# Kernel optimization log

Measured on AMD Instinct MI355X. Metric: run time of the kernel, lower is better.

Reference implementation:

```python
import jax, jax.numpy as jnp
import numpy as np

NUM_EMB = 81920
EMB_DIM = 64


def setup_inputs() -> dict:
    key = jax.random.key(0)
    k1, k2 = jax.random.split(key)
    z = jax.random.normal(k1, (4, 8, 8, 8, EMB_DIM), dtype=jnp.float32)
    # faithful to nn.Embedding init: uniform(-1/K, 1/K)
    emb = jax.random.uniform(k2, (NUM_EMB, EMB_DIM), dtype=jnp.float32,
                             minval=-1.0 / NUM_EMB, maxval=1.0 / NUM_EMB)
    return {"z": z, "emb": emb}


def reference(z, emb):
    bs, h, w, d, c = z.shape
    zf = z.reshape(-1, c)  # [N, C]
    # squared euclidean distances; argmin identical to cdist argmin
    # [N, K] = ||z||^2 - 2 z.E^T + ||E||^2
    d2 = (jnp.sum(zf * zf, axis=-1, keepdims=True)
          - 2.0 * jnp.einsum('nc,kc->nk', zf, emb)
          + jnp.sum(emb * emb, axis=-1))
    idx = jnp.argmin(d2, axis=1)  # [N]
    quantized = emb[idx].reshape(bs, h, w, d, c)
    commitment_loss = jnp.mean((z - jax.lax.stop_gradient(quantized)) ** 2)
    vq_loss = jnp.mean((quantized - jax.lax.stop_gradient(z)) ** 2)
    quantized_st = z + jax.lax.stop_gradient(quantized - z)
    return quantized_st, vq_loss, commitment_loss, idx.reshape(bs, h, w, d)
```

## Files before the change

kernel.cpp:

```cpp
#include <hip/hip_runtime.h>
#include <stdint.h>

#define NQ 2048
#define KK 81920
#define CD 64
#define CAP 64
#define DMARG 1.6e-5f
#define QPB 64
#define NQBLK 32
#define NSLICE 160
#define SPX 20
#define SPB 5

#define OUT_VQ 131072
#define OUT_CM 131073
#define OUT_IDX 131074

#define WS_CNT  8192
#define WS_LOSS 32768
#define WS_CAND 33024
#define WS_ZBF  589824
#define WS_EBF  851968
#define WS_BMAX 11337728

typedef short v8s __attribute__((ext_vector_type(8)));
typedef float v4f __attribute__((ext_vector_type(4)));

__device__ __forceinline__ unsigned int f2o(float f) {
  unsigned int u = __float_as_uint(f);
  return (u & 0x80000000u) ? ~u : (u | 0x80000000u);
}
__device__ __forceinline__ float o2f(unsigned int u) {
  unsigned int v = (u & 0x80000000u) ? (u & 0x7FFFFFFFu) : ~u;
  return __uint_as_float(v);
}
__device__ __forceinline__ unsigned int bf16rne(float f) {
  unsigned int u = __float_as_uint(f);
  u = u + 0x7FFFu + ((u >> 16) & 1u);
  return u >> 16;
}

#define NZ4 32768
#define NTOT4 1343488
__global__ __launch_bounds__(256) void convert_kernel(
    const float* __restrict__ z, const float* __restrict__ emb,
    unsigned int* __restrict__ zbf, unsigned int* __restrict__ ebf,
    int* __restrict__ cnt, float* __restrict__ loss) {
  const int gid = blockIdx.x * 256 + threadIdx.x;
  if (gid < NQ) cnt[gid] = 0;
  if (gid == NQ) *loss = 0.0f;
  const int stride = gridDim.x * 256;
#pragma unroll 1
  for (int i = gid; i < NTOT4; i += stride) {
    const bool isz = (i < NZ4);
    const float4 v = isz ? ((const float4*)z)[i] : ((const float4*)emb)[i - NZ4];
    uint2 o;
    o.x = bf16rne(v.x) | (bf16rne(v.y) << 16);
    o.y = bf16rne(v.z) | (bf16rne(v.w) << 16);
    if (isz) ((uint2*)zbf)[i] = o;
    else     ((uint2*)ebf)[i - NZ4] = o;
  }
}

struct BlkMap { int q0, slice0, xcd, sgrp; };
__device__ __forceinline__ BlkMap decode_block(int bid) {
  BlkMap m;
  m.xcd = bid & 7;
  const int i = bid >> 3;
  const int qblk = i & 31;
  m.sgrp = i >> 5;
  m.q0 = qblk * QPB;
  m.slice0 = m.xcd * SPX + m.sgrp * SPB;
  return m;
}

__device__ __forceinline__ void load_B4(v8s (&Bb)[4][2],
                                        const unsigned short* __restrict__ ebf,
                                        int code0, int lrow, int quad) {
#pragma unroll
  for (int cg = 0; cg < 4; ++cg) {
    const unsigned short* er = ebf + (size_t)(code0 + cg * 16 + lrow) * CD + quad * 8;
    Bb[cg][0] = *(const v8s*)er;
    Bb[cg][1] = *(const v8s*)(er + 32);
  }
}

__global__ __launch_bounds__(256, 2) void pass1_kernel(
    const unsigned short* __restrict__ zbf, const unsigned short* __restrict__ ebf,
    unsigned int* __restrict__ bmax) {
  const int tid = threadIdx.x;
  const int wave = tid >> 6, lane = tid & 63;
  const int quad = lane >> 4, lrow = lane & 15;
  const BlkMap bm = decode_block(blockIdx.x);

  v8s A0[4], A1[4];
#pragma unroll
  for (int qg = 0; qg < 4; ++qg) {
    const unsigned short* zr = zbf + (size_t)(bm.q0 + qg * 16 + lrow) * CD + quad * 8;
    A0[qg] = *(const v8s*)zr;
    A1[qg] = *(const v8s*)(zr + 32);
  }

  float pmax[4][4];
#pragma unroll
  for (int qg = 0; qg < 4; ++qg)
#pragma unroll
    for (int r = 0; r < 4; ++r) pmax[qg][r] = -1e30f;

#pragma unroll 1
  for (int s = 0; s < SPB; ++s) {
#pragma unroll 1
    for (int h = 0; h < 2; ++h) {
      v8s B[4][2];
      load_B4(B, ebf, (bm.slice0 + s) * 512 + wave * 128 + h * 64, lrow, quad);
#pragma unroll
      for (int qg = 0; qg < 4; ++qg) {
#pragma unroll
        for (int cg = 0; cg < 4; ++cg) {
          v4f acc = {0.f, 0.f, 0.f, 0.f};
          acc = __builtin_amdgcn_mfma_f32_16x16x32_bf16(A0[qg], B[cg][0], acc, 0, 0, 0);
          acc = __builtin_amdgcn_mfma_f32_16x16x32_bf16(A1[qg], B[cg][1], acc, 0, 0, 0);
#pragma unroll
          for (int r = 0; r < 4; ++r) pmax[qg][r] = fmaxf(pmax[qg][r], acc[r]);
        }
      }
    }
  }

#pragma unroll
  for (int m = 1; m <= 8; m <<= 1)
#pragma unroll
    for (int qg = 0; qg < 4; ++qg)
#pragma unroll
      for (int r = 0; r < 4; ++r)
        pmax[qg][r] = fmaxf(pmax[qg][r], __shfl_xor(pmax[qg][r], m, 64));

  __shared__ unsigned int smax[4][QPB];
  if (lrow == 0) {
#pragma unroll
    for (int qg = 0; qg < 4; ++qg) {
      uint4 v;
      v.x = f2o(pmax[qg][0]); v.y = f2o(pmax[qg][1]);
      v.z = f2o(pmax[qg][2]); v.w = f2o(pmax[qg][3]);
      *(uint4*)&smax[wave][qg * 16 + quad * 4] = v;
    }
  }
  __syncthreads();
  if (tid < QPB) {
    unsigned int m0 = smax[0][tid], m1 = smax[1][tid];
    unsigned int m2 = smax[2][tid], m3 = smax[3][tid];
    unsigned int m01 = m0 > m1 ? m0 : m1;
    unsigned int m23 = m2 > m3 ? m2 : m3;
    bmax[(size_t)(bm.q0 + tid) * 32 + bm.xcd * 4 + bm.sgrp] = m01 > m23 ? m01 : m23;
  }
}

__global__ __launch_bounds__(256, 2) void collect_kernel(
    const unsigned short* __restrict__ zbf, const unsigned short* __restrict__ ebf,
    const unsigned int* __restrict__ bmax, int* __restrict__ cnt,
    int* __restrict__ cand) {
  const int tid = threadIdx.x;
  const int wave = tid >> 6, lane = tid & 63;
  const int quad = lane >> 4, lrow = lane & 15;
  const BlkMap bm = decode_block(blockIdx.x);

  __shared__ unsigned int qmaxl[QPB];
  if (tid < QPB) {
    const uint4* bp = (const uint4*)(bmax + (size_t)(bm.q0 + tid) * 32);
    unsigned int m = 0;
#pragma unroll
    for (int j = 0; j < 8; ++j) {
      uint4 v = bp[j];
      unsigned int a = v.x > v.y ? v.x : v.y;
      unsigned int b = v.z > v.w ? v.z : v.w;
      unsigned int c = a > b ? a : b;
      m = m > c ? m : c;
    }
    qmaxl[tid] = m;
  }

  v8s A0[4], A1[4];
#pragma unroll
  for (int qg = 0; qg < 4; ++qg) {
    const unsigned short* zr = zbf + (size_t)(bm.q0 + qg * 16 + lrow) * CD + quad * 8;
    A0[qg] = *(const v8s*)zr;
    A1[qg] = *(const v8s*)(zr + 32);
  }
  __syncthreads();
  float thr[4][4];
#pragma unroll
  for (int qg = 0; qg < 4; ++qg) {
    const uint4 tv = *(const uint4*)&qmaxl[qg * 16 + quad * 4];
    thr[qg][0] = o2f(tv.x) - DMARG; thr[qg][1] = o2f(tv.y) - DMARG;
    thr[qg][2] = o2f(tv.z) - DMARG; thr[qg][3] = o2f(tv.w) - DMARG;
  }

#pragma unroll 1
  for (int s = 0; s < SPB; ++s) {
#pragma unroll 1
    for (int h = 0; h < 2; ++h) {
      const int code0 = (bm.slice0 + s) * 512 + wave * 128 + h * 64;
      v8s B[4][2];
      load_B4(B, ebf, code0, lrow, quad);
#pragma unroll
      for (int qg = 0; qg < 4; ++qg) {
#pragma unroll
        for (int cg = 0; cg < 4; ++cg) {
          v4f acc = {0.f, 0.f, 0.f, 0.f};
          acc = __builtin_amdgcn_mfma_f32_16x16x32_bf16(A0[qg], B[cg][0], acc, 0, 0, 0);
          acc = __builtin_amdgcn_mfma_f32_16x16x32_bf16(A1[qg], B[cg][1], acc, 0, 0, 0);
          const float m01 = fmaxf(acc[0] - thr[qg][0], acc[1] - thr[qg][1]);
          const float m23 = fmaxf(acc[2] - thr[qg][2], acc[3] - thr[qg][3]);
          if (fmaxf(m01, m23) >= 0.0f) {
            const int code = code0 + cg * 16 + lrow;
#pragma unroll
            for (int r = 0; r < 4; ++r) {
              if (acc[r] >= thr[qg][r]) {
                const int q = bm.q0 + qg * 16 + quad * 4 + r;
                const int pos = atomicAdd(&cnt[q], 1);
                if (pos < CAP) cand[q * CAP + pos] = code;
              }
            }
          }
        }
      }
    }
  }
}

__device__ __forceinline__ unsigned long long exact_key(
    const float* __restrict__ emb, const float zr[CD], float zn2, int k) {
#pragma clang fp contract(off)
  float er[CD];
  const float4* ep = (const float4*)(emb + (size_t)k * CD);
#pragma unroll
  for (int j = 0; j < 16; ++j) {
    float4 v = ep[j];
    er[4 * j] = v.x; er[4 * j + 1] = v.y; er[4 * j + 2] = v.z; er[4 * j + 3] = v.w;
  }
  float acc[16];
#pragma unroll
  for (int j = 0; j < 16; ++j) acc[j] = 0.0f;
#pragma unroll
  for (int q4 = 0; q4 < 16; ++q4) {
    const int jb = 4 * (q4 & 3), cb = 4 * q4;
    acc[jb + 0] = __builtin_fmaf(er[cb + 0], zr[cb + 0], acc[jb + 0]);
    acc[jb + 1] = __builtin_fmaf(er[cb + 1], zr[cb + 1], acc[jb + 1]);
    acc[jb + 2] = __builtin_fmaf(er[cb + 2], zr[cb + 2], acc[jb + 2]);
    acc[jb + 3] = __builtin_fmaf(er[cb + 3], zr[cb + 3], acc[jb + 3]);
  }
  float b8[8], b4[4];
#pragma unroll
  for (int j = 0; j < 8; ++j) b8[j] = acc[j] + acc[j + 8];
#pragma unroll
  for (int j = 0; j < 4; ++j) b4[j] = b8[j] + b8[j + 4];
  const float dot = (b4[0] + b4[2]) + (b4[1] + b4[3]);
  const float t = zn2 - 2.0f * dot;
  return ((unsigned long long)f2o(t) << 32) | (unsigned int)k;
}

__global__ __launch_bounds__(256) void rescore_finalize_kernel(
    const float* __restrict__ z, const float* __restrict__ emb,
    const int* __restrict__ cnt, const int* __restrict__ cand,
    float* __restrict__ out, float* __restrict__ loss) {
#pragma clang fp contract(off)
  const int t = threadIdx.x;
  const int wv = t >> 6, lane = t & 63;
  const int n = blockIdx.x * 4 + wv;

  float zr[CD];
  {
    const float4* zp = (const float4*)(z + (size_t)n * CD);
#pragma unroll
    for (int i = 0; i < 16; ++i) {
      float4 v = zp[i];
      zr[4 * i] = v.x; zr[4 * i + 1] = v.y; zr[4 * i + 2] = v.z; zr[4 * i + 3] = v.w;
    }
  }
  float zn2;
  {
    float r[8];
#pragma unroll
    for (int j = 0; j < 8; ++j) r[j] = zr[j] * zr[j];
#pragma unroll
    for (int i = 8; i < CD; i += 8)
#pragma unroll
      for (int j = 0; j < 8; ++j) r[j] += zr[i + j] * zr[i + j];
    zn2 = ((r[0] + r[1]) + (r[2] + r[3])) + ((r[4] + r[5]) + (r[6] + r[7]));
  }

  const int c = cnt[n];
  unsigned long long best = ~0ull;
  if (c <= CAP) {
    if (lane < c) best = exact_key(emb, zr, zn2, cand[n * CAP + lane]);
  } else {
#pragma unroll 1
    for (int k = lane; k < KK; k += 64) {
      unsigned long long key = exact_key(emb, zr, zn2, k);
      best = (key < best) ? key : best;
    }
  }
#pragma unroll
  for (int m = 32; m; m >>= 1) {
    unsigned long long o = __shfl_xor(best, m, 64);
    best = (o < best) ? o : best;
  }
  const int idx = (int)(best & 0xFFFFFFFFull);

  const float e = emb[(size_t)idx * CD + lane];
  const float zv = z[(size_t)n * CD + lane];
  const float dst = e - zv;
  out[(size_t)n * CD + lane] = zv + dst;
  if (lane == 0) out[OUT_IDX + n] = (float)idx;
  float d = zv - e;
  float sq = d * d;
#pragma unroll
  for (int off = 32; off > 0; off >>= 1) sq += __shfl_down(sq, off, 64);
  __shared__ float part[4];
  if (lane == 0) part[wv] = sq;
  __syncthreads();
  if (t == 0) atomicAdd(loss, part[0] + part[1] + part[2] + part[3]);
}

__global__ void write_losses(const float* __restrict__ loss, float* __restrict__ out) {
  float m = *loss / (float)(NQ * CD);
  out[OUT_VQ] = m;
  out[OUT_CM] = m;
}

extern "C" void kernel_launch(void* const* d_in, const int* in_sizes, int n_in,
                              void* d_out, int out_size, void* d_ws, size_t ws_size,
                              hipStream_t stream) {
  const float* z = (const float*)d_in[0];
  const float* emb = (const float*)d_in[1];
  float* out = (float*)d_out;
  char* ws = (char*)d_ws;
  int* cnt = (int*)(ws + WS_CNT);
  float* loss = (float*)(ws + WS_LOSS);
  int* cand = (int*)(ws + WS_CAND);
  unsigned int* zbf = (unsigned int*)(ws + WS_ZBF);
  unsigned int* ebf = (unsigned int*)(ws + WS_EBF);
  unsigned int* bmax = (unsigned int*)(ws + WS_BMAX);

  convert_kernel<<<1312, 256, 0, stream>>>(z, emb, zbf, ebf, cnt, loss);
  const int nblk = NQBLK * (NSLICE / SPB);
  pass1_kernel<<<nblk, 256, 0, stream>>>(
      (const unsigned short*)zbf, (const unsigned short*)ebf, bmax);
  collect_kernel<<<nblk, 256, 0, stream>>>(
      (const unsigned short*)zbf, (const unsigned short*)ebf, bmax, cnt, cand);
  rescore_finalize_kernel<<<NQ / 4, 256, 0, stream>>>(z, emb, cnt, cand, out, loss);
  write_losses<<<1, 1, 0, stream>>>(loss, out);
}
```

Baseline: 174.1 us.

## Replace collect pass with per-chunk max and chunk-level exact rescoring

```diff
diff --git a/kernel.cpp b/kernel.cpp
--- a/kernel.cpp
+++ b/kernel.cpp
@@ -4,24 +4,22 @@
 #define NQ 2048
 #define KK 81920
 #define CD 64
-#define CAP 64
 #define DMARG 1.6e-5f
 #define QPB 64
 #define NQBLK 32
-#define NSLICE 160
 #define SPX 20
 #define SPB 5
+#define NCHUNK 640
 
 #define OUT_VQ 131072
 #define OUT_CM 131073
 #define OUT_IDX 131074
 
-#define WS_CNT  8192
-#define WS_LOSS 32768
-#define WS_CAND 33024
-#define WS_ZBF  589824
-#define WS_EBF  851968
-#define WS_BMAX 11337728
+#define WS_LOSS 0
+#define WS_TICKET 256
+#define WS_ZBF  1024
+#define WS_EBF  263168
+#define WS_CMAX 10748928
 
 typedef short v8s __attribute__((ext_vector_type(8)));
 typedef float v4f __attribute__((ext_vector_type(4)));
@@ -45,10 +43,9 @@
 __global__ __launch_bounds__(256) void convert_kernel(
     const float* __restrict__ z, const float* __restrict__ emb,
     unsigned int* __restrict__ zbf, unsigned int* __restrict__ ebf,
-    int* __restrict__ cnt, float* __restrict__ loss) {
+    float* __restrict__ loss, unsigned int* __restrict__ ticket) {
   const int gid = blockIdx.x * 256 + threadIdx.x;
-  if (gid < NQ) cnt[gid] = 0;
-  if (gid == NQ) *loss = 0.0f;
+  if (gid == 0) { *loss = 0.0f; *ticket = 0u; }
   const int stride = gridDim.x * 256;
 #pragma unroll 1
   for (int i = gid; i < NTOT4; i += stride) {
@@ -62,15 +59,15 @@
   }
 }
 
-struct BlkMap { int q0, slice0, xcd, sgrp; };
+struct BlkMap { int q0, slice0; };
 __device__ __forceinline__ BlkMap decode_block(int bid) {
   BlkMap m;
-  m.xcd = bid & 7;
+  const int xcd = bid & 7;
   const int i = bid >> 3;
   const int qblk = i & 31;
-  m.sgrp = i >> 5;
+  const int sgrp = i >> 5;
   m.q0 = qblk * QPB;
-  m.slice0 = m.xcd * SPX + m.sgrp * SPB;
+  m.slice0 = xcd * SPX + sgrp * SPB;
   return m;
 }
 
@@ -87,7 +84,7 @@
 
 __global__ __launch_bounds__(256, 2) void pass1_kernel(
     const unsigned short* __restrict__ zbf, const unsigned short* __restrict__ ebf,
-    unsigned int* __restrict__ bmax) {
+    unsigned int* __restrict__ cmax) {
   const int tid = threadIdx.x;
   const int wave = tid >> 6, lane = tid & 63;
   const int quad = lane >> 4, lrow = lane & 15;
@@ -101,14 +98,14 @@
     A1[qg] = *(const v8s*)(zr + 32);
   }
 
-  float pmax[4][4];
-#pragma unroll
-  for (int qg = 0; qg < 4; ++qg)
-#pragma unroll
-    for (int r = 0; r < 4; ++r) pmax[qg][r] = -1e30f;
-
 #pragma unroll 1
   for (int s = 0; s < SPB; ++s) {
+    float pmax[4][4];
+#pragma unroll
+    for (int qg = 0; qg < 4; ++qg)
+#pragma unroll
+      for (int r = 0; r < 4; ++r) pmax[qg][r] = -1e30f;
+
 #pragma unroll 1
     for (int h = 0; h < 2; ++h) {
       v8s B[4][2];
@@ -125,105 +122,23 @@
         }
       }
     }
-  }
-
-#pragma unroll
-  for (int m = 1; m <= 8; m <<= 1)
-#pragma unroll
-    for (int qg = 0; qg < 4; ++qg)
-#pragma unroll
-      for (int r = 0; r < 4; ++r)
-        pmax[qg][r] = fmaxf(pmax[qg][r], __shfl_xor(pmax[qg][r], m, 64));
-
-  __shared__ unsigned int smax[4][QPB];
-  if (lrow == 0) {
-#pragma unroll
-    for (int qg = 0; qg < 4; ++qg) {
-      uint4 v;
-      v.x = f2o(pmax[qg][0]); v.y = f2o(pmax[qg][1]);
-      v.z = f2o(pmax[qg][2]); v.w = f2o(pmax[qg][3]);
-      *(uint4*)&smax[wave][qg * 16 + quad * 4] = v;
-    }
-  }
-  __syncthreads();
-  if (tid < QPB) {
-    unsigned int m0 = smax[0][tid], m1 = smax[1][tid];
-    unsigned int m2 = smax[2][tid], m3 = smax[3][tid];
-    unsigned int m01 = m0 > m1 ? m0 : m1;
-    unsigned int m23 = m2 > m3 ? m2 : m3;
-    bmax[(size_t)(bm.q0 + tid) * 32 + bm.xcd * 4 + bm.sgrp] = m01 > m23 ? m01 : m23;
-  }
-}
-
-__global__ __launch_bounds__(256, 2) void collect_kernel(
-    const unsigned short* __restrict__ zbf, const unsigned short* __restrict__ ebf,
-    const unsigned int* __restrict__ bmax, int* __restrict__ cnt,
-    int* __restrict__ cand) {
-  const int tid = threadIdx.x;
-  const int wave = tid >> 6, lane = tid & 63;
-  const int quad = lane >> 4, lrow = lane & 15;
-  const BlkMap bm = decode_block(blockIdx.x);
-
-  __shared__ unsigned int qmaxl[QPB];
-  if (tid < QPB) {
-    const uint4* bp = (const uint4*)(bmax + (size_t)(bm.q0 + tid) * 32);
-    unsigned int m = 0;
-#pragma unroll
-    for (int j = 0; j < 8; ++j) {
-      uint4 v = bp[j];
-      unsigned int a = v.x > v.y ? v.x : v.y;
-      unsigned int b = v.z > v.w ? v.z : v.w;
-      unsigned int c = a > b ? a : b;
-      m = m > c ? m : c;
-    }
-    qmaxl[tid] = m;
-  }
-
-  v8s A0[4], A1[4];
-#pragma unroll
-  for (int qg = 0; qg < 4; ++qg) {
-    const unsigned short* zr = zbf + (size_t)(bm.q0 + qg * 16 + lrow) * CD + quad * 8;
-    A0[qg] = *(const v8s*)zr;
-    A1[qg] = *(const v8s*)(zr + 32);
-  }
-  __syncthreads();
-  float thr[4][4];
-#pragma unroll
-  for (int qg = 0; qg < 4; ++qg) {
-    const uint4 tv = *(const uint4*)&qmaxl[qg * 16 + quad * 4];
-    thr[qg][0] = o2f(tv.x) - DMARG; thr[qg][1] = o2f(tv.y) - DMARG;
-    thr[qg][2] = o2f(tv.z) - DMARG; thr[qg][3] = o2f(tv.w) - DMARG;
-  }
-
-#pragma unroll 1
-  for (int s = 0; s < SPB; ++s) {
-#pragma unroll 1
-    for (int h = 0; h < 2; ++h) {
-      const int code0 = (bm.slice0 + s) * 512 + wave * 128 + h * 64;
-      v8s B[4][2];
-      load_B4(B, ebf, code0, lrow, quad);
-#pragma unroll
-      for (int qg = 0; qg < 4; ++qg) {
-#pragma unroll
-        for (int cg = 0; cg < 4; ++cg) {
-          v4f acc = {0.f, 0.f, 0.f, 0.f};
-          acc = __builtin_amdgcn_mfma_f32_16x16x32_bf16(A0[qg], B[cg][0], acc, 0, 0, 0);
-          acc = __builtin_amdgcn_mfma_f32_16x16x32_bf16(A1[qg], B[cg][1], acc, 0, 0, 0);
-          const float m01 = fmaxf(acc[0] - thr[qg][0], acc[1] - thr[qg][1]);
-          const float m23 = fmaxf(acc[2] - thr[qg][2], acc[3] - thr[qg][3]);
-          if (fmaxf(m01, m23) >= 0.0f) {
-            const int code = code0 + cg * 16 + lrow;
-#pragma unroll
-            for (int r = 0; r < 4; ++r) {
-              if (acc[r] >= thr[qg][r]) {
-                const int q = bm.q0 + qg * 16 + quad * 4 + r;
-                const int pos = atomicAdd(&cnt[q], 1);
-                if (pos < CAP) cand[q * CAP + pos] = code;
-              }
-            }
-          }
-        }
-      }
+
+#pragma unroll
+    for (int m = 1; m <= 8; m <<= 1)
+#pragma unroll
+      for (int qg = 0; qg < 4; ++qg)
+#pragma unroll
+        for (int r = 0; r < 4; ++r)
+          pmax[qg][r] = fmaxf(pmax[qg][r], __shfl_xor(pmax[qg][r], m, 64));
+
+    const int ch = (bm.slice0 + s) * 4 + wave;
+    if (lrow == 0) {
+#pragma unroll
+      for (int qg = 0; qg < 4; ++qg)
+#pragma unroll
+        for (int r = 0; r < 4; ++r)
+          cmax[(size_t)(bm.q0 + qg * 16 + quad * 4 + r) * NCHUNK + ch] =
+              f2o(pmax[qg][r]);
     }
   }
 }
@@ -261,8 +176,8 @@
 
 __global__ __launch_bounds__(256) void rescore_finalize_kernel(
     const float* __restrict__ z, const float* __restrict__ emb,
-    const int* __restrict__ cnt, const int* __restrict__ cand,
-    float* __restrict__ out, float* __restrict__ loss) {
+    const unsigned int* __restrict__ cmax, float* __restrict__ out,
+    float* __restrict__ loss, unsigned int* __restrict__ ticket) {
 #pragma clang fp contract(off)
   const int t = threadIdx.x;
   const int wv = t >> 6, lane = t & 63;
@@ -289,15 +204,32 @@
     zn2 = ((r[0] + r[1]) + (r[2] + r[3])) + ((r[4] + r[5]) + (r[6] + r[7]));
   }
 
-  const int c = cnt[n];
+  const unsigned int* cm = cmax + (size_t)n * NCHUNK;
+  unsigned int val[10];
+#pragma unroll
+  for (int j = 0; j < 10; ++j) val[j] = cm[j * 64 + lane];
+  unsigned int qm = val[0];
+#pragma unroll
+  for (int j = 1; j < 10; ++j) qm = val[j] > qm ? val[j] : qm;
+#pragma unroll
+  for (int m = 32; m; m >>= 1) {
+    unsigned int o = (unsigned int)__shfl_xor((int)qm, m, 64);
+    qm = o > qm ? o : qm;
+  }
+  const float thr = o2f(qm) - DMARG;
+
   unsigned long long best = ~0ull;
-  if (c <= CAP) {
-    if (lane < c) best = exact_key(emb, zr, zn2, cand[n * CAP + lane]);
-  } else {
-#pragma unroll 1
-    for (int k = lane; k < KK; k += 64) {
-      unsigned long long key = exact_key(emb, zr, zn2, k);
-      best = (key < best) ? key : best;
+#pragma unroll 1
+  for (int j = 0; j < 10; ++j) {
+    unsigned long long mask = __ballot(o2f(val[j]) >= thr);
+    while (mask) {
+      const int b = __ffsll((long long)mask) - 1;
+      mask &= mask - 1;
+      const int c0 = (j * 64 + b) * 128;
+      unsigned long long k1 = exact_key(emb, zr, zn2, c0 + lane);
+      unsigned long long k2 = exact_key(emb, zr, zn2, c0 + 64 + lane);
+      best = (k1 < best) ? k1 : best;
+      best = (k2 < best) ? k2 : best;
     }
   }
 #pragma unroll
@@ -319,13 +251,16 @@
   __shared__ float part[4];
   if (lane == 0) part[wv] = sq;
   __syncthreads();
-  if (t == 0) atomicAdd(loss, part[0] + part[1] + part[2] + part[3]);
-}
-
-__global__ void write_losses(const float* __restrict__ loss, float* __restrict__ out) {
-  float m = *loss / (float)(NQ * CD);
-  out[OUT_VQ] = m;
-  out[OUT_CM] = m;
+  if (t == 0) {
+    atomicAdd(loss, part[0] + part[1] + part[2] + part[3]);
+    __threadfence();
+    const unsigned int tk = atomicAdd(ticket, 1u);
+    if (tk == gridDim.x - 1) {
+      const float m = atomicAdd(loss, 0.0f) / (float)(NQ * CD);
+      out[OUT_VQ] = m;
+      out[OUT_CM] = m;
+    }
+  }
 }
 
 extern "C" void kernel_launch(void* const* d_in, const int* in_sizes, int n_in,
@@ -335,19 +270,15 @@
   const float* emb = (const float*)d_in[1];
   float* out = (float*)d_out;
   char* ws = (char*)d_ws;
-  int* cnt = (int*)(ws + WS_CNT);
   float* loss = (float*)(ws + WS_LOSS);
-  int* cand = (int*)(ws + WS_CAND);
+  unsigned int* ticket = (unsigned int*)(ws + WS_TICKET);
   unsigned int* zbf = (unsigned int*)(ws + WS_ZBF);
   unsigned int* ebf = (unsigned int*)(ws + WS_EBF);
-  unsigned int* bmax = (unsigned int*)(ws + WS_BMAX);
-
-  convert_kernel<<<1312, 256, 0, stream>>>(z, emb, zbf, ebf, cnt, loss);
-  const int nblk = NQBLK * (NSLICE / SPB);
+  unsigned int* cmaxp = (unsigned int*)(ws + WS_CMAX);
+
+  convert_kernel<<<1312, 256, 0, stream>>>(z, emb, zbf, ebf, loss, ticket);
+  const int nblk = NQBLK * 32;
   pass1_kernel<<<nblk, 256, 0, stream>>>(
-      (const unsigned short*)zbf, (const unsigned short*)ebf, bmax);
-  collect_kernel<<<nblk, 256, 0, stream>>>(
-      (const unsigned short*)zbf, (const unsigned short*)ebf, bmax, cnt, cand);
-  rescore_finalize_kernel<<<NQ / 4, 256, 0, stream>>>(z, emb, cnt, cand, out, loss);
-  write_losses<<<1, 1, 0, stream>>>(loss, out);
-}
+      (const unsigned short*)zbf, (const unsigned short*)ebf, cmaxp);
+  rescore_finalize_kernel<<<NQ / 4, 256, 0, stream>>>(z, emb, cmaxp, out, loss, ticket);
+}
```

Measured after the change: 220.1 us. 26.5% more time.
